# Optimization experiments

Measured on AMD Instinct MI355X. Metric: run time of the kernel, lower is better.

Reference implementation:

```python
import jax, jax.numpy as jnp
import numpy as np

N_NODES = 100000
N_EDGES = 1600000
C = 64


def _spline_conv(x, src, dst, u, w, root, bias, n_nodes):
    """SplineConv, dim=1, kernel_size=2, degree=1, open spline, aggr='mean'.

    For K=2, degree=1, pseudo u in [0,1]: basis = (1-u) on knot 0, u on knot 1.
    message_e = (1-u_e) * x[src_e] @ w[0] + u_e * x[src_e] @ w[1]
    Compute the two GEMMs at node level (N < E) then gather, which is
    mathematically identical and cheaper.
    """
    h0 = x @ w[0]  # [N, C]
    h1 = x @ w[1]  # [N, C]
    uc = u[:, None]  # [E, 1]
    msg = (1.0 - uc) * h0[src] + uc * h1[src]  # [E, C]
    agg = jax.ops.segment_sum(msg, dst, num_segments=n_nodes)  # [N, C]
    deg = jax.ops.segment_sum(jnp.ones_like(u), dst, num_segments=n_nodes)
    agg = agg / jnp.maximum(deg, 1.0)[:, None]  # mean aggregation
    return agg + x @ root + bias


def setup_inputs() -> dict:
    key = jax.random.key(0)
    ks = jax.random.split(key, 10)
    x = jax.random.normal(ks[0], (N_NODES, C), dtype=jnp.float32)
    edge_index = jax.random.randint(ks[1], (2, N_EDGES), 0, N_NODES, dtype=jnp.int64)
    edge_attr = jax.random.uniform(ks[2], (N_EDGES, 1), dtype=jnp.float32)
    s = 1.0 / np.sqrt(C)
    w1 = jax.random.uniform(ks[3], (2, C, C), jnp.float32, -s, s)
    root1 = jax.random.uniform(ks[4], (C, C), jnp.float32, -s, s)
    b1 = jnp.zeros((C,), jnp.float32)
    w2 = jax.random.uniform(ks[5], (2, C, C), jnp.float32, -s, s)
    root2 = jax.random.uniform(ks[6], (C, C), jnp.float32, -s, s)
    b2 = jnp.zeros((C,), jnp.float32)
    return {"x": x, "edge_index": edge_index, "edge_attr": edge_attr,
            "w1": w1, "root1": root1, "b1": b1,
            "w2": w2, "root2": root2, "b2": b2}


def reference(x, edge_index, edge_attr, w1, root1, b1, w2, root2, b2):
    src, dst = edge_index[0], edge_index[1]
    u = edge_attr[:, 0]
    n = x.shape[0]
    h = _spline_conv(x, src, dst, u, w1, root1, b1, n)
    h = _spline_conv(h, src, dst, u, w2, root2, b2, n)
    return h
```

## Files before the change

kernel.cpp:

```cpp
#include <hip/hip_runtime.h>

#define CDIM 64

typedef __attribute__((ext_vector_type(8))) short bf16x8;
typedef __attribute__((ext_vector_type(4))) float f32x4;

__device__ __forceinline__ short bf16r(float f) {
    unsigned a = __float_as_uint(f);
    a = (a + 0x7fffu + ((a >> 16) & 1u)) >> 16;
    return (short)a;
}
__device__ __forceinline__ unsigned bfpack(float lo, float hi) {
    unsigned a = __float_as_uint(lo);
    a = (a + 0x7fffu + ((a >> 16) & 1u)) >> 16;
    unsigned b = __float_as_uint(hi);
    b = (b + 0x7fffu + ((b >> 16) & 1u)) & 0xffff0000u;
    return a | b;
}

__global__ __launch_bounds__(256) void k_pack(const float* __restrict__ x,
                                              unsigned* __restrict__ xb32, size_t n2) {
    size_t t = (size_t)blockIdx.x * 256 + threadIdx.x;
    size_t stride = (size_t)gridDim.x * 256;
    for (size_t i = t; i < n2; i += stride) {
        float2 v = ((const float2*)x)[i];
        xb32[i] = bfpack(v.x, v.y);
    }
}

#define NPB_SHIFT 9
#define BKN (1 << NPB_SHIFT)
#define BPAD 10240
#define PART_CH 2048

__global__ __launch_bounds__(256) void k_prep(int* __restrict__ bkt_cursor, int n_buckets,
                                              const float* __restrict__ w1,
                                              const float* __restrict__ root1,
                                              const float* __restrict__ w2,
                                              const float* __restrict__ root2,
                                              short* __restrict__ wtg) {
    int tid = threadIdx.x;
    if (blockIdx.x == 0) {
        if (tid < n_buckets) bkt_cursor[tid] = tid * BPAD;
        return;
    }
    int l = blockIdx.x - 1;
    const float* s0 = l ? w2 : w1;
    const float* srcs[3] = {s0, s0 + 4096, l ? root2 : root1};
    short* o = wtg + (size_t)l * 3 * 4096;
    for (int i = tid; i < 12288; i += 256) {
        int m = i >> 12, r = i & 4095, k = r >> 6, n = r & 63;
        o[(m << 12) + (n << 6) + k] = bf16r(srcs[m][r]);
    }
}

__global__ __launch_bounds__(256) void k_part(const int* __restrict__ src,
                                              const int* __restrict__ dst,
                                              const float* __restrict__ u,
                                              int* __restrict__ bkt_cursor,
                                              unsigned long long* __restrict__ rec,
                                              int n_edges, int n_buckets) {
    __shared__ int cnt_s[256];
    __shared__ int off_s[256];
    int tid = threadIdx.x;
    cnt_s[tid] = 0;
    __syncthreads();
    int e0 = blockIdx.x * PART_CH + tid * 8;
    int d[8], s[8];
    float uu[8];
    if (e0 + 8 <= n_edges) {
        int4 d0 = *(const int4*)(dst + e0), d1 = *(const int4*)(dst + e0 + 4);
        int4 s0 = *(const int4*)(src + e0), s1 = *(const int4*)(src + e0 + 4);
        float4 u0 = *(const float4*)(u + e0), u1 = *(const float4*)(u + e0 + 4);
        d[0]=d0.x; d[1]=d0.y; d[2]=d0.z; d[3]=d0.w; d[4]=d1.x; d[5]=d1.y; d[6]=d1.z; d[7]=d1.w;
        s[0]=s0.x; s[1]=s0.y; s[2]=s0.z; s[3]=s0.w; s[4]=s1.x; s[5]=s1.y; s[6]=s1.z; s[7]=s1.w;
        uu[0]=u0.x; uu[1]=u0.y; uu[2]=u0.z; uu[3]=u0.w; uu[4]=u1.x; uu[5]=u1.y; uu[6]=u1.z; uu[7]=u1.w;
    } else {
#pragma unroll
        for (int i = 0; i < 8; ++i) {
            int e = e0 + i;
            bool ok = e < n_edges;
            d[i] = ok ? dst[e] : -1;
            s[i] = ok ? src[e] : 0;
            uu[i] = ok ? u[e] : 0.f;
        }
    }
#pragma unroll
    for (int i = 0; i < 8; ++i)
        if (d[i] >= 0) atomicAdd(&cnt_s[d[i] >> NPB_SHIFT], 1);
    __syncthreads();
    if (tid < n_buckets) {
        int c = cnt_s[tid];
        off_s[tid] = c ? atomicAdd(&bkt_cursor[tid], c) : 0;
    }
    __syncthreads();
#pragma unroll
    for (int i = 0; i < 8; ++i) {
        if (d[i] >= 0) {
            int b = d[i] >> NPB_SHIFT;
            int p = atomicAdd(&off_s[b], 1);
            unsigned uq = (unsigned)(uu[i] * 32767.0f + 0.5f);
            rec[p] = ((unsigned long long)(unsigned)d[i] << 32)
                   | (unsigned long long)(((unsigned)s[i] << 15) | uq);
        }
    }
}

__global__ __launch_bounds__(256) void k_bscan(const int* __restrict__ bkt_cursor,
                                               int* __restrict__ ebase,
                                               int* __restrict__ row_start,
                                               int n_buckets, int n_nodes) {
    __shared__ int sm[256];
    int tid = threadIdx.x;
    int v = (tid < n_buckets) ? (bkt_cursor[tid] - tid * BPAD) : 0;
    sm[tid] = v;
    __syncthreads();
    for (int off = 1; off < 256; off <<= 1) {
        int t = (tid >= off) ? sm[tid - off] : 0;
        __syncthreads();
        sm[tid] += t;
        __syncthreads();
    }
    if (tid < n_buckets) ebase[tid] = sm[tid] - v;
    if (tid == 255) row_start[n_nodes] = sm[255];
}

__global__ __launch_bounds__(1024) void k_scat2(const unsigned long long* __restrict__ rec,
                                                const int* __restrict__ bkt_cursor,
                                                const int* __restrict__ ebase,
                                                int* __restrict__ row_start,
                                                unsigned* __restrict__ em32,
                                                int n_nodes) {
    __shared__ int cnt_s[BKN];
    __shared__ int sc_s[BKN];
    int tid = threadIdx.x;
    int b = blockIdx.x;
    int lo = b << NPB_SHIFT;
    int nrec = bkt_cursor[b] - b * BPAD;
    const unsigned long long* r0 = rec + (size_t)b * BPAD;
    int eb = ebase[b];

    if (tid < BKN) cnt_s[tid] = 0;
    __syncthreads();
    for (int i = tid; i < nrec; i += 1024) {
        int d = (int)(r0[i] >> 32) - lo;
        atomicAdd(&cnt_s[d], 1);
    }
    __syncthreads();
    if (tid < BKN) sc_s[tid] = cnt_s[tid];
    __syncthreads();
    for (int off = 1; off < BKN; off <<= 1) {
        int t = 0;
        if (tid < BKN && tid >= off) t = sc_s[tid - off];
        __syncthreads();
        if (tid < BKN) sc_s[tid] += t;
        __syncthreads();
    }
    if (tid < BKN) {
        int excl = sc_s[tid] - cnt_s[tid];
        int node = lo + tid;
        if (node < n_nodes) row_start[node] = eb + excl;
        cnt_s[tid] = excl;
    }
    __syncthreads();
    for (int i = tid; i < nrec; i += 1024) {
        unsigned long long r = r0[i];
        int d = (int)(r >> 32) - lo;
        int p = atomicAdd(&cnt_s[d], 1);
        em32[eb + p] = (unsigned)r;
    }
}

__global__ __launch_bounds__(256) void k_fused(
        const unsigned* __restrict__ xb_in,
        const unsigned* __restrict__ em32,
        const int* __restrict__ row_start,
        const short* __restrict__ wb,
        const float* __restrict__ bias,
        float* __restrict__ out,
        unsigned short* __restrict__ xb_out,
        int n_nodes) {
    __shared__ __align__(16) unsigned gl[64][68];
    int wave = threadIdx.x >> 6;
    int lane = threadIdx.x & 63;
    int q = lane >> 4;
    int ql = lane & 15;
    int nodew = blockIdx.x * 64 + wave * 16;
    const float inv15 = 1.0f / 32767.0f;

    for (int t = 0; t < 4; ++t) {
        int n = nodew + q * 4 + t;
        bool nok = n < n_nodes;
        int start = nok ? row_start[n] : 0;
        int end = nok ? row_start[n + 1] : 0;
        float a0 = 0.f, a1 = 0.f, a2 = 0.f, a3 = 0.f;
        float b0 = 0.f, b1 = 0.f, b2 = 0.f, b3 = 0.f;
        int j = start;
        for (; j + 4 <= end; j += 4) {
            unsigned e[4];
            uint2 v[4];
#pragma unroll
            for (int i = 0; i < 4; ++i) e[i] = em32[j + i];
#pragma unroll
            for (int i = 0; i < 4; ++i)
                v[i] = *(const uint2*)(xb_in + (size_t)(e[i] >> 15) * 32 + 2 * ql);
#pragma unroll
            for (int i = 0; i < 4; ++i) {
                float uu = (float)(e[i] & 0x7fffu) * inv15;
                float wa = 1.0f - uu;
                float c0 = __uint_as_float(v[i].x << 16);
                float c1 = __uint_as_float(v[i].x & 0xffff0000u);
                float c2 = __uint_as_float(v[i].y << 16);
                float c3 = __uint_as_float(v[i].y & 0xffff0000u);
                a0 += wa * c0; a1 += wa * c1; a2 += wa * c2; a3 += wa * c3;
                b0 += uu * c0; b1 += uu * c1; b2 += uu * c2; b3 += uu * c3;
            }
        }
        if (j < end) {
            unsigned e[4];
            uint2 v[4];
            float m[4];
#pragma unroll
            for (int i = 0; i < 4; ++i) {
                int idx = j + i;
                bool ok = idx < end;
                e[i] = em32[ok ? idx : (end - 1)];
                m[i] = ok ? 1.0f : 0.0f;
            }
#pragma unroll
            for (int i = 0; i < 4; ++i)
                v[i] = *(const uint2*)(xb_in + (size_t)(e[i] >> 15) * 32 + 2 * ql);
#pragma unroll
            for (int i = 0; i < 4; ++i) {
                float uu = (float)(e[i] & 0x7fffu) * inv15;
                float wa = (1.0f - uu) * m[i], wu = uu * m[i];
                float c0 = __uint_as_float(v[i].x << 16);
                float c1 = __uint_as_float(v[i].x & 0xffff0000u);
                float c2 = __uint_as_float(v[i].y << 16);
                float c3 = __uint_as_float(v[i].y & 0xffff0000u);
                a0 += wa * c0; a1 += wa * c1; a2 += wa * c2; a3 += wa * c3;
                b0 += wu * c0; b1 += wu * c1; b2 += wu * c2; b3 += wu * c3;
            }
        }
        float s = 1.0f / fmaxf((float)(end - start), 1.0f);
        int row = wave * 16 + q * 4 + t;
        *(uint2*)&gl[row][2 * ql] = make_uint2(bfpack(a0 * s, a1 * s), bfpack(a2 * s, a3 * s));
        *(uint2*)&gl[row][32 + 2 * ql] = make_uint2(bfpack(b0 * s, b1 * s), bfpack(b2 * s, b3 * s));
    }

    int quad = lane >> 4;
    int m16 = lane & 15;
    int arow = nodew + m16;
    const short* gp = (const short*)&gl[wave * 16 + m16][0];
    const unsigned* xp = xb_in + (size_t)arow * 32;
    bf16x8 zf = {0, 0, 0, 0, 0, 0, 0, 0};
    bf16x8 aG0[2], aG1[2], aX[2];
#pragma unroll
    for (int kf = 0; kf < 2; ++kf) {
        aG0[kf] = *(const bf16x8*)(gp + kf * 32 + quad * 8);
        aG1[kf] = *(const bf16x8*)(gp + 64 + kf * 32 + quad * 8);
        aX[kf] = (arow < n_nodes) ? *(const bf16x8*)(xp + kf * 16 + quad * 4) : zf;
    }
#pragma unroll
    for (int nt = 0; nt < 4; ++nt) {
        f32x4 acc = {0.f, 0.f, 0.f, 0.f};
#pragma unroll
        for (int kf = 0; kf < 2; ++kf) {
            int col = nt * 16 + m16;
            bf16x8 bw0 = *(const bf16x8*)(wb + (col << 6) + kf * 32 + quad * 8);
            bf16x8 bw1 = *(const bf16x8*)(wb + ((64 + col) << 6) + kf * 32 + quad * 8);
            bf16x8 bwR = *(const bf16x8*)(wb + ((128 + col) << 6) + kf * 32 + quad * 8);
            acc = __builtin_amdgcn_mfma_f32_16x16x32_bf16(aG0[kf], bw0, acc, 0, 0, 0);
            acc = __builtin_amdgcn_mfma_f32_16x16x32_bf16(aG1[kf], bw1, acc, 0, 0, 0);
            acc = __builtin_amdgcn_mfma_f32_16x16x32_bf16(aX[kf], bwR, acc, 0, 0, 0);
        }
        float bcol = bias[nt * 16 + m16];
#pragma unroll
        for (int r = 0; r < 4; ++r) {
            int node = nodew + quad * 4 + r;
            if (node < n_nodes) {
                size_t off = (size_t)node * CDIM + nt * 16 + m16;
                float o = acc[r] + bcol;
                if (out) out[off] = o;
                if (xb_out) xb_out[off] = (unsigned short)bf16r(o);
            }
        }
    }
}

extern "C" void kernel_launch(void* const* d_in, const int* in_sizes, int n_in,
                              void* d_out, int out_size, void* d_ws, size_t ws_size,
                              hipStream_t stream) {
    const float* x = (const float*)d_in[0];
    const int* edge_index = (const int*)d_in[1];
    const float* edge_attr = (const float*)d_in[2];
    const float* w1 = (const float*)d_in[3];
    const float* root1 = (const float*)d_in[4];
    const float* b1 = (const float*)d_in[5];
    const float* w2 = (const float*)d_in[6];
    const float* root2 = (const float*)d_in[7];
    const float* b2 = (const float*)d_in[8];

    int n_nodes = in_sizes[0] / CDIM;
    int n_edges = in_sizes[2];
    const int* src = edge_index;
    const int* dst = edge_index + n_edges;

    size_t F = (size_t)n_nodes * CDIM;
    unsigned* xbA = (unsigned*)d_ws;
    unsigned* xbB = xbA + F / 2;
    unsigned* em32 = xbB + F / 2;
    int* row_start = (int*)(em32 + n_edges);
    int n_buckets = (n_nodes + BKN - 1) >> NPB_SHIFT;
    int* ebase = row_start + n_nodes + 1;
    int* bkt_cursor = ebase + n_buckets;
    uintptr_t p = (uintptr_t)(bkt_cursor + n_buckets);
    p = (p + 15) & ~(uintptr_t)15;
    short* wtg = (short*)p;
    p += (size_t)2 * 3 * 4096 * sizeof(short);
    p = (p + 15) & ~(uintptr_t)15;
    unsigned long long* rec = (unsigned long long*)p;
    float* out = (float*)d_out;

    int gB = (n_nodes + 63) / 64;
    int gP = (n_edges + PART_CH - 1) / PART_CH;

    k_pack<<<2048, 256, 0, stream>>>(x, xbA, F / 2);
    k_prep<<<3, 256, 0, stream>>>(bkt_cursor, n_buckets, w1, root1, w2, root2, wtg);
    k_part<<<gP, 256, 0, stream>>>(src, dst, edge_attr, bkt_cursor, rec, n_edges, n_buckets);
    k_bscan<<<1, 256, 0, stream>>>(bkt_cursor, ebase, row_start, n_buckets, n_nodes);
    k_scat2<<<n_buckets, 1024, 0, stream>>>(rec, bkt_cursor, ebase, row_start, em32, n_nodes);

    k_fused<<<gB, 256, 0, stream>>>(xbA, em32, row_start, wtg, b1,
                                    nullptr, (unsigned short*)xbB, n_nodes);
    k_fused<<<gB, 256, 0, stream>>>(xbB, em32, row_start, wtg + 3 * 4096, b2,
                                    out, nullptr, n_nodes);
}
```

Before: 268.3 us.

## Stage partition records in LDS, split bucket scatter into sub-blocks, unroll gather by 8

The partition kernel now does a block-local prefix scan over bucket counts and stages its records in shared memory, then writes them out in bucket-contiguous order so global stores coalesce. The per-bucket CSR scatter is split into 8 sub-blocks of 64 nodes each. Each sub-block rescans the whole bucket but touches only its own nodes, which gives more parallelism at the cost of redundant reads. The fused gather loop is unrolled from 4 to 8 edges to keep more loads in flight, which raises register pressure.

```diff
diff --git a/kernel.cpp b/kernel.cpp
--- a/kernel.cpp
+++ b/kernel.cpp
@@ -61,7 +61,12 @@
                                               unsigned long long* __restrict__ rec,
                                               int n_edges, int n_buckets) {
     __shared__ int cnt_s[256];
-    __shared__ int off_s[256];
+    __shared__ int excl_s[256];
+    __shared__ int cur_s[256];
+    __shared__ int goff_s[256];
+    __shared__ int tot_s;
+    __shared__ unsigned long long rec_s[PART_CH];
+    __shared__ int tgt_s[PART_CH];
     int tid = threadIdx.x;
     cnt_s[tid] = 0;
     __syncthreads();
@@ -89,21 +94,37 @@
     for (int i = 0; i < 8; ++i)
         if (d[i] >= 0) atomicAdd(&cnt_s[d[i] >> NPB_SHIFT], 1);
     __syncthreads();
-    if (tid < n_buckets) {
-        int c = cnt_s[tid];
-        off_s[tid] = c ? atomicAdd(&bkt_cursor[tid], c) : 0;
-    }
+    int c = cnt_s[tid];
+    excl_s[tid] = c;
+    __syncthreads();
+    for (int off = 1; off < 256; off <<= 1) {
+        int t = (tid >= off) ? excl_s[tid - off] : 0;
+        __syncthreads();
+        excl_s[tid] += t;
+        __syncthreads();
+    }
+    int excl = excl_s[tid] - c;
+    if (tid == 255) tot_s = excl_s[255];
+    __syncthreads();
+    excl_s[tid] = excl;
+    cur_s[tid] = excl;
+    goff_s[tid] = (tid < n_buckets && c) ? atomicAdd(&bkt_cursor[tid], c) : 0;
     __syncthreads();
 #pragma unroll
     for (int i = 0; i < 8; ++i) {
         if (d[i] >= 0) {
             int b = d[i] >> NPB_SHIFT;
-            int p = atomicAdd(&off_s[b], 1);
+            int p = atomicAdd(&cur_s[b], 1);
             unsigned uq = (unsigned)(uu[i] * 32767.0f + 0.5f);
-            rec[p] = ((unsigned long long)(unsigned)d[i] << 32)
-                   | (unsigned long long)(((unsigned)s[i] << 15) | uq);
-        }
-    }
+            rec_s[p] = ((unsigned long long)(unsigned)d[i] << 32)
+                     | (unsigned long long)(((unsigned)s[i] << 15) | uq);
+            tgt_s[p] = goff_s[b] + (p - excl_s[b]);
+        }
+    }
+    __syncthreads();
+    int tot = tot_s;
+    for (int i = tid; i < tot; i += 256)
+        rec[tgt_s[i]] = rec_s[i];
 }
 
 __global__ __launch_bounds__(256) void k_bscan(const int* __restrict__ bkt_cursor,
@@ -125,49 +146,57 @@
     if (tid == 255) row_start[n_nodes] = sm[255];
 }
 
-__global__ __launch_bounds__(1024) void k_scat2(const unsigned long long* __restrict__ rec,
-                                                const int* __restrict__ bkt_cursor,
-                                                const int* __restrict__ ebase,
-                                                int* __restrict__ row_start,
-                                                unsigned* __restrict__ em32,
-                                                int n_nodes) {
-    __shared__ int cnt_s[BKN];
-    __shared__ int sc_s[BKN];
+#define SUBS 8
+__global__ __launch_bounds__(256) void k_scat2(const unsigned long long* __restrict__ rec,
+                                               const int* __restrict__ bkt_cursor,
+                                               const int* __restrict__ ebase,
+                                               int* __restrict__ row_start,
+                                               unsigned* __restrict__ em32,
+                                               int n_nodes) {
+    __shared__ int cnt_s[64];
+    __shared__ int sc_s[64];
+    __shared__ int below_s;
     int tid = threadIdx.x;
-    int b = blockIdx.x;
-    int lo = b << NPB_SHIFT;
+    int b = blockIdx.x >> 3;
+    int sub = blockIdx.x & 7;
+    int lo = (b << NPB_SHIFT) + (sub << 6);
     int nrec = bkt_cursor[b] - b * BPAD;
     const unsigned long long* r0 = rec + (size_t)b * BPAD;
-    int eb = ebase[b];
-
-    if (tid < BKN) cnt_s[tid] = 0;
-    __syncthreads();
-    for (int i = tid; i < nrec; i += 1024) {
-        int d = (int)(r0[i] >> 32) - lo;
-        atomicAdd(&cnt_s[d], 1);
-    }
-    __syncthreads();
-    if (tid < BKN) sc_s[tid] = cnt_s[tid];
-    __syncthreads();
-    for (int off = 1; off < BKN; off <<= 1) {
-        int t = 0;
-        if (tid < BKN && tid >= off) t = sc_s[tid - off];
-        __syncthreads();
-        if (tid < BKN) sc_s[tid] += t;
-        __syncthreads();
-    }
-    if (tid < BKN) {
+    if (tid < 64) cnt_s[tid] = 0;
+    if (tid == 0) below_s = 0;
+    __syncthreads();
+    int below = 0;
+    for (int i = tid; i < nrec; i += 256) {
+        int d = (int)(r0[i] >> 32);
+        int rel = d - lo;
+        if (d < lo) below++;
+        else if (rel < 64) atomicAdd(&cnt_s[rel], 1);
+    }
+    if (below) atomicAdd(&below_s, below);
+    __syncthreads();
+    if (tid < 64) sc_s[tid] = cnt_s[tid];
+    __syncthreads();
+    for (int off = 1; off < 64; off <<= 1) {
+        int t = (tid < 64 && tid >= off) ? sc_s[tid - off] : 0;
+        __syncthreads();
+        if (tid < 64) sc_s[tid] += t;
+        __syncthreads();
+    }
+    int base = ebase[b] + below_s;
+    if (tid < 64) {
         int excl = sc_s[tid] - cnt_s[tid];
         int node = lo + tid;
-        if (node < n_nodes) row_start[node] = eb + excl;
+        if (node < n_nodes) row_start[node] = base + excl;
         cnt_s[tid] = excl;
     }
     __syncthreads();
-    for (int i = tid; i < nrec; i += 1024) {
+    for (int i = tid; i < nrec; i += 256) {
         unsigned long long r = r0[i];
-        int d = (int)(r >> 32) - lo;
-        int p = atomicAdd(&cnt_s[d], 1);
-        em32[eb + p] = (unsigned)r;
+        int rel = (int)(r >> 32) - lo;
+        if ((unsigned)rel < 64u) {
+            int p = atomicAdd(&cnt_s[rel], 1);
+            em32[base + p] = (unsigned)r;
+        }
     }
 }
 
@@ -196,16 +225,16 @@
         float a0 = 0.f, a1 = 0.f, a2 = 0.f, a3 = 0.f;
         float b0 = 0.f, b1 = 0.f, b2 = 0.f, b3 = 0.f;
         int j = start;
-        for (; j + 4 <= end; j += 4) {
-            unsigned e[4];
-            uint2 v[4];
-#pragma unroll
-            for (int i = 0; i < 4; ++i) e[i] = em32[j + i];
-#pragma unroll
-            for (int i = 0; i < 4; ++i)
+        for (; j + 8 <= end; j += 8) {
+            unsigned e[8];
+            uint2 v[8];
+#pragma unroll
+            for (int i = 0; i < 8; ++i) e[i] = em32[j + i];
+#pragma unroll
+            for (int i = 0; i < 8; ++i)
                 v[i] = *(const uint2*)(xb_in + (size_t)(e[i] >> 15) * 32 + 2 * ql);
 #pragma unroll
-            for (int i = 0; i < 4; ++i) {
+            for (int i = 0; i < 8; ++i) {
                 float uu = (float)(e[i] & 0x7fffu) * inv15;
                 float wa = 1.0f - uu;
                 float c0 = __uint_as_float(v[i].x << 16);
@@ -217,21 +246,21 @@
             }
         }
         if (j < end) {
-            unsigned e[4];
-            uint2 v[4];
-            float m[4];
-#pragma unroll
-            for (int i = 0; i < 4; ++i) {
+            unsigned e[8];
+            uint2 v[8];
+            float m[8];
+#pragma unroll
+            for (int i = 0; i < 8; ++i) {
                 int idx = j + i;
                 bool ok = idx < end;
                 e[i] = em32[ok ? idx : (end - 1)];
                 m[i] = ok ? 1.0f : 0.0f;
             }
 #pragma unroll
-            for (int i = 0; i < 4; ++i)
+            for (int i = 0; i < 8; ++i)
                 v[i] = *(const uint2*)(xb_in + (size_t)(e[i] >> 15) * 32 + 2 * ql);
 #pragma unroll
-            for (int i = 0; i < 4; ++i) {
+            for (int i = 0; i < 8; ++i) {
                 float uu = (float)(e[i] & 0x7fffu) * inv15;
                 float wa = (1.0f - uu) * m[i], wu = uu * m[i];
                 float c0 = __uint_as_float(v[i].x << 16);
@@ -329,7 +358,7 @@
     k_prep<<<3, 256, 0, stream>>>(bkt_cursor, n_buckets, w1, root1, w2, root2, wtg);
     k_part<<<gP, 256, 0, stream>>>(src, dst, edge_attr, bkt_cursor, rec, n_edges, n_buckets);
     k_bscan<<<1, 256, 0, stream>>>(bkt_cursor, ebase, row_start, n_buckets, n_nodes);
-    k_scat2<<<n_buckets, 1024, 0, stream>>>(rec, bkt_cursor, ebase, row_start, em32, n_nodes);
+    k_scat2<<<n_buckets * SUBS, 256, 0, stream>>>(rec, bkt_cursor, ebase, row_start, em32, n_nodes);
 
     k_fused<<<gB, 256, 0, stream>>>(xbA, em32, row_start, wtg, b1,
                                     nullptr, (unsigned short*)xbB, n_nodes);
```

Measured after the change: 292.8 us. +9.1%, slower.
